# Kernel optimization log

Hardware: AMD Instinct MI355X
Metric: run time of the kernel (lower is better)

The kernel has to match this reference:

```python
import jax, jax.numpy as jnp
import numpy as np

D_MODEL = 1024
N_HEADS = 16
N_KV = 4
HD = D_MODEL // N_HEADS  # 64
N_REP = N_HEADS // N_KV
WINDOW = 128
SCALE = HD ** -0.5
B, T = 2, 2048


def _rope(x):
    # x: [B, H, T, hd]; half-split rotate_half RoPE, base 10000
    t = x.shape[2]
    hd = x.shape[-1]
    inv_freq = 1.0 / (10000.0 ** (jnp.arange(0, hd, 2, dtype=jnp.float32) / hd))
    freqs = jnp.arange(t, dtype=jnp.float32)[:, None] * inv_freq[None, :]  # [T, hd/2]
    cos = jnp.cos(freqs)[None, None]  # [1,1,T,hd/2]
    sin = jnp.sin(freqs)[None, None]
    x1, x2 = x[..., : hd // 2], x[..., hd // 2:]
    return jnp.concatenate([x1 * cos - x2 * sin, x1 * sin + x2 * cos], axis=-1)


def setup_inputs() -> dict:
    key = jax.random.key(0)
    ks = jax.random.split(key, 6)
    s = 0.02
    return {
        "query": jax.random.normal(ks[0], (B, T, D_MODEL), dtype=jnp.float32),
        "Wq": jax.random.normal(ks[1], (D_MODEL, D_MODEL), dtype=jnp.float32) * s,
        "Wk": jax.random.normal(ks[2], (N_KV * HD, D_MODEL), dtype=jnp.float32) * s,
        "Wv": jax.random.normal(ks[3], (N_KV * HD, D_MODEL), dtype=jnp.float32) * s,
        "W1": jax.random.normal(ks[4], (4 * D_MODEL, D_MODEL), dtype=jnp.float32) * s,
        "W2": jax.random.normal(ks[5], (D_MODEL, 4 * D_MODEL), dtype=jnp.float32) * s,
    }


def reference(query, Wq, Wk, Wv, W1, W2):
    b, t, _ = query.shape
    # QKV projections (nn.Linear, no bias): x @ W.T
    q = (query @ Wq.T).reshape(b, t, N_HEADS, HD).transpose(0, 2, 1, 3)  # [B,H,T,hd]
    k = (query @ Wk.T).reshape(b, t, N_KV, HD).transpose(0, 2, 1, 3)    # [B,Hkv,T,hd]
    v = (query @ Wv.T).reshape(b, t, N_KV, HD).transpose(0, 2, 1, 3)
    # Rotary embeddings on q/k (self-attention)
    q = _rope(q)
    k = _rope(k)
    # GQA: repeat kv heads (kv-head-major ordering, matches torch expand+reshape)
    k = jnp.repeat(k, N_REP, axis=1)
    v = jnp.repeat(v, N_REP, axis=1)
    # scores + causal sliding-window band mask (True = masked)
    scores = jnp.einsum("bhqd,bhkd->bhqk", q, k) * SCALE
    i = jnp.arange(t)[:, None]
    j = jnp.arange(t)[None, :]
    mask = (j > i) | (j < i - (WINDOW - 1))  # causal window of size WINDOW
    scores = jnp.where(mask[None, None], jnp.float32(-1e30), scores)
    attn = jax.nn.softmax(scores, axis=-1)
    out = jnp.einsum("bhqk,bhkd->bhqd", attn, v)
    out = out.transpose(0, 2, 1, 3).reshape(b, t, D_MODEL)
    # out_proj: Linear(d,4d) -> SiLU -> Linear(4d,d)
    h = out @ W1.T
    h = h * jax.nn.sigmoid(h)
    return h @ W2.T
```

## Files before the change

kernel.cpp:

```cpp
#include <hip/hip_runtime.h>
#include <math.h>


typedef __bf16 bf16x8 __attribute__((ext_vector_type(8)));
typedef __bf16 bf16x4 __attribute__((ext_vector_type(4)));
typedef float  f32x4  __attribute__((ext_vector_type(4)));

extern __shared__ __align__(16) char smem[];

#define GLOAD_LDS16(g, l) __builtin_amdgcn_global_load_lds(               \
    (const __attribute__((address_space(1))) void*)(g),                   \
    (__attribute__((address_space(3))) void*)(l), 16, 0, 0)

__device__ __forceinline__ unsigned pk2(float a, float b) {
    union { __bf16 h[2]; unsigned u; } t;
    t.h[0] = (__bf16)a; t.h[1] = (__bf16)b;
    return t.u;
}

__global__ __launch_bounds__(256) void MultiAttention_60722247631706_conv(
    const float* x, const float* Wq, const float* Wk, const float* Wv,
    const float* W1, const float* W2, float* out, float* ws, int phase)
{
    __bf16* xbf    = (__bf16*)(ws + 6291456);
    __bf16* wqkvbf = (__bf16*)(ws + 8388608);
    __bf16* w1bf   = (__bf16*)(ws + 10485760);
    __bf16* w2bf   = (__bf16*)(ws + 8388608);
    const int tid = threadIdx.x;

    if (phase == 5) {
        const long long total4 = 9961472 / 4;
        for (long long i4 = (long long)blockIdx.x * 256 + tid; i4 < total4;
             i4 += (long long)gridDim.x * 256) {
            const long long i = i4 * 4;
            const float* src; __bf16* dst;
            if (i < 4194304)      { src = x  + i;             dst = xbf    + i; }
            else if (i < 5242880) { src = Wq + (i - 4194304); dst = wqkvbf + (i - 4194304); }
            else if (i < 5505024) { src = Wk + (i - 5242880); dst = wqkvbf + (i - 4194304); }
            else if (i < 5767168) { src = Wv + (i - 5505024); dst = wqkvbf + (i - 4194304); }
            else                  { src = W1 + (i - 5767168); dst = w1bf   + (i - 5767168); }
            const f32x4 v = *(const f32x4*)src;
            bf16x4 o;
            o[0] = (__bf16)v[0]; o[1] = (__bf16)v[1];
            o[2] = (__bf16)v[2]; o[3] = (__bf16)v[3];
            *(bf16x4*)dst = o;
        }
    } else {
        const long long total4 = 4194304 / 4;
        for (long long i4 = (long long)blockIdx.x * 256 + tid; i4 < total4;
             i4 += (long long)gridDim.x * 256) {
            const long long i = i4 * 4;
            const f32x4 v = *(const f32x4*)(W2 + i);
            bf16x4 o;
            o[0] = (__bf16)v[0]; o[1] = (__bf16)v[1];
            o[2] = (__bf16)v[2]; o[3] = (__bf16)v[3];
            *(bf16x4*)(w2bf + i) = o;
        }
        const f32x4 z = {0.f, 0.f, 0.f, 0.f};
        for (long long i4 = (long long)blockIdx.x * 256 + tid; i4 < total4;
             i4 += (long long)gridDim.x * 256) {
            *(f32x4*)(out + i4 * 4) = z;
        }
    }
}

__global__ __launch_bounds__(256) void MultiAttention_60722247631706_attn(
    float* ws)
{
    const float* Y = ws;
    __bf16* obf = (__bf16*)(ws + 8388608);

    __bf16* Ks = (__bf16*)smem;
    __bf16* Vt = Ks + 192 * 72;

    const int qt  = blockIdx.x & 31;
    const int kvh = (blockIdx.x >> 5) & 3;
    const int b   = blockIdx.x >> 7;
    const int q0  = qt * 64;
    const int wb  = q0 - 128;

    const int tid  = threadIdx.x;
    const int w    = tid >> 6;
    const int lane = tid & 63;
    const int l16  = lane & 15;
    const int quad = lane >> 4;
    const int h    = kvh * 4 + w;

    const float* Yb = Y + (size_t)b * 2048 * 1536;

    for (int i = tid; i < 192 * 8; i += 256) {
        const int r  = i >> 3;
        const int c8 = (i & 7) * 8;
        const int j  = wb + r;
        bf16x8 kv;
        if (j >= 0) {
            const float* kp = Yb + (size_t)j * 1536 + 1024 + kvh * 64 + c8;
            const f32x4 a = *(const f32x4*)kp;
            const f32x4 c = *(const f32x4*)(kp + 4);
            kv[0] = (__bf16)a[0]; kv[1] = (__bf16)a[1];
            kv[2] = (__bf16)a[2]; kv[3] = (__bf16)a[3];
            kv[4] = (__bf16)c[0]; kv[5] = (__bf16)c[1];
            kv[6] = (__bf16)c[2]; kv[7] = (__bf16)c[3];
        } else {
            const __bf16 z = (__bf16)0.f;
            kv[0]=z; kv[1]=z; kv[2]=z; kv[3]=z; kv[4]=z; kv[5]=z; kv[6]=z; kv[7]=z;
        }
        *(bf16x8*)(Ks + r * 72 + c8) = kv;
    }
    for (int i = tid; i < 192 * 16; i += 256) {
        const int r  = i >> 4;
        const int c4 = (i & 15) * 4;
        const int j  = wb + r;
        f32x4 vv = {0.f, 0.f, 0.f, 0.f};
        if (j >= 0) vv = *(const f32x4*)(Yb + (size_t)j * 1536 + 1280 + kvh * 64 + c4);
        Vt[(c4 + 0) * 200 + r] = (__bf16)vv[0];
        Vt[(c4 + 1) * 200 + r] = (__bf16)vv[1];
        Vt[(c4 + 2) * 200 + r] = (__bf16)vv[2];
        Vt[(c4 + 3) * 200 + r] = (__bf16)vv[3];
    }

    bf16x8 qf[4][2];
#pragma unroll
    for (int qn = 0; qn < 4; ++qn)
#pragma unroll
        for (int kk = 0; kk < 2; ++kk) {
            const float* qp = Yb + (size_t)(q0 + qn * 16 + l16) * 1536
                              + h * 64 + kk * 32 + quad * 8;
            const f32x4 a = *(const f32x4*)qp;
            const f32x4 c = *(const f32x4*)(qp + 4);
            bf16x8 t;
            t[0] = (__bf16)(a[0] * 0.125f); t[1] = (__bf16)(a[1] * 0.125f);
            t[2] = (__bf16)(a[2] * 0.125f); t[3] = (__bf16)(a[3] * 0.125f);
            t[4] = (__bf16)(c[0] * 0.125f); t[5] = (__bf16)(c[1] * 0.125f);
            t[6] = (__bf16)(c[2] * 0.125f); t[7] = (__bf16)(c[3] * 0.125f);
            qf[qn][kk] = t;
        }

    __syncthreads();

    f32x4 oacc[4][4];
#pragma unroll
    for (int qm = 0; qm < 4; ++qm)
#pragma unroll
        for (int dn = 0; dn < 4; ++dn) {
            f32x4 z = {0.f, 0.f, 0.f, 0.f};
            oacc[qm][dn] = z;
        }
    float m_run[4] = {-1e30f, -1e30f, -1e30f, -1e30f};
    float l_run[4] = {0.f, 0.f, 0.f, 0.f};

    const int kclip = -wb;

    for (int kb = 0; kb < 3; ++kb) {
        f32x4 s[4][4];
#pragma unroll
        for (int km = 0; km < 4; ++km)
#pragma unroll
            for (int qn = 0; qn < 4; ++qn) {
                f32x4 z = {0.f, 0.f, 0.f, 0.f};
                s[km][qn] = z;
            }
#pragma unroll
        for (int kk = 0; kk < 2; ++kk) {
            bf16x8 kf[4];
#pragma unroll
            for (int km = 0; km < 4; ++km)
                kf[km] = *(const bf16x8*)(Ks + (kb * 64 + km * 16 + l16) * 72
                                          + kk * 32 + quad * 8);
#pragma unroll
            for (int km = 0; km < 4; ++km)
#pragma unroll
                for (int qn = 0; qn < 4; ++qn)
                    s[km][qn] = __builtin_amdgcn_mfma_f32_16x16x32_bf16(
                        kf[km], qf[qn][kk], s[km][qn], 0, 0, 0);
        }

        unsigned cu[4][4][2];
        float corr[4];
#pragma unroll
        for (int qn = 0; qn < 4; ++qn) {
            float mx = -1e30f;
#pragma unroll
            for (int km = 0; km < 4; ++km)
#pragma unroll
                for (int r = 0; r < 4; ++r) {
                    const int kl  = kb * 64 + km * 16 + quad * 4 + r;
                    const int dlt = kl - (qn * 16 + l16);
                    const bool ok = (dlt >= 1) && (dlt <= 128) && (kl >= kclip);
                    const float sv = ok ? s[km][qn][r] : -1e30f;
                    s[km][qn][r] = sv;
                    mx = fmaxf(mx, sv);
                }
            mx = fmaxf(mx, __shfl_xor(mx, 16));
            mx = fmaxf(mx, __shfl_xor(mx, 32));
            const float mnew = fmaxf(fmaxf(m_run[qn], mx), -1e20f);
            corr[qn] = expf(m_run[qn] - mnew);
            m_run[qn] = mnew;
            float rowsum = 0.f;
#pragma unroll
            for (int km = 0; km < 4; ++km) {
#pragma unroll
                for (int r = 0; r < 4; ++r) {
                    const float p = expf(s[km][qn][r] - mnew);
                    s[km][qn][r] = p;
                    rowsum += p;
                }
                cu[qn][km][0] = pk2(s[km][qn][0], s[km][qn][1]);
                cu[qn][km][1] = pk2(s[km][qn][2], s[km][qn][3]);
            }
            rowsum += __shfl_xor(rowsum, 16);
            rowsum += __shfl_xor(rowsum, 32);
            l_run[qn] = l_run[qn] * corr[qn] + rowsum;
        }

#pragma unroll
        for (int qm = 0; qm < 4; ++qm)
#pragma unroll
            for (int r = 0; r < 4; ++r) {
                const float f = __shfl(corr[qm], (lane & 48) | (quad * 4 + r));
                oacc[qm][0][r] *= f; oacc[qm][1][r] *= f;
                oacc[qm][2][r] *= f; oacc[qm][3][r] *= f;
            }

#pragma unroll
        for (int kk = 0; kk < 2; ++kk) {
            bf16x8 vf[4];
#pragma unroll
            for (int dn = 0; dn < 4; ++dn)
                vf[dn] = *(const bf16x8*)(Vt + (dn * 16 + l16) * 200
                                          + kb * 64 + kk * 32 + quad * 8);
            const int srcA = ((quad & 1) * 32) + l16;
            const int hi   = quad >> 1;
#pragma unroll
            for (int qm = 0; qm < 4; ++qm) {
                const unsigned a0 = (unsigned)__shfl((int)cu[qm][2*kk  ][0], srcA);
                const unsigned a1 = (unsigned)__shfl((int)cu[qm][2*kk  ][1], srcA);
                const unsigned b0 = (unsigned)__shfl((int)cu[qm][2*kk+1][0], srcA);
                const unsigned b1 = (unsigned)__shfl((int)cu[qm][2*kk+1][1], srcA);
                const unsigned c0 = (unsigned)__shfl((int)cu[qm][2*kk  ][0], srcA + 16);
                const unsigned c1 = (unsigned)__shfl((int)cu[qm][2*kk  ][1], srcA + 16);
                const unsigned d0 = (unsigned)__shfl((int)cu[qm][2*kk+1][0], srcA + 16);
                const unsigned d1 = (unsigned)__shfl((int)cu[qm][2*kk+1][1], srcA + 16);
                union { unsigned u[4]; bf16x8 v; } af;
                af.u[0] = hi ? b0 : a0;
                af.u[1] = hi ? b1 : a1;
                af.u[2] = hi ? d0 : c0;
                af.u[3] = hi ? d1 : c1;
#pragma unroll
                for (int dn = 0; dn < 4; ++dn)
                    oacc[qm][dn] = __builtin_amdgcn_mfma_f32_16x16x32_bf16(
                        af.v, vf[dn], oacc[qm][dn], 0, 0, 0);
            }
        }
    }

#pragma unroll
    for (int qm = 0; qm < 4; ++qm) {
        const float rl = 1.f / l_run[qm];
#pragma unroll
        for (int r = 0; r < 4; ++r) {
            const float f = __shfl(rl, (lane & 48) | (quad * 4 + r));
            const int q = q0 + qm * 16 + quad * 4 + r;
            __bf16* op = obf + ((size_t)(b * 2048 + q)) * 1024 + h * 64 + l16;
#pragma unroll
            for (int dn = 0; dn < 4; ++dn)
                op[dn * 16] = (__bf16)(oacc[qm][dn][r] * f);
        }
    }
}

__global__ __launch_bounds__(256) void MultiAttention_60722247631706_kernel(
    float* out, float* ws, int phase)
{
    float*  Y      = ws;
    __bf16* xbf    = (__bf16*)(ws + 6291456);
    __bf16* wqkvbf = (__bf16*)(ws + 8388608);
    __bf16* w1bf   = (__bf16*)(ws + 10485760);
    __bf16* obf    = (__bf16*)(ws + 8388608);
    __bf16* hbf    = (__bf16*)ws;
    __bf16* w2bf   = (__bf16*)(ws + 8388608);

    const int tid = threadIdx.x;

    __bf16* As = (__bf16*)smem;
    __bf16* Bs = As + 128 * 64;

    const __bf16* Ap; const __bf16* Bp; int lda, ldb, ntn, kbase;
    int bid = blockIdx.x;
    if (phase == 0) {
        Ap = xbf; lda = 1024; Bp = wqkvbf; ldb = 1024; ntn = 12; kbase = 0;
    } else if (phase == 3) {
        Ap = obf; lda = 1024; Bp = w1bf;   ldb = 1024; ntn = 32; kbase = 0;
    } else {
        const int ks = bid >> 8;  bid &= 255;
        Ap = hbf; lda = 4096; Bp = w2bf;   ldb = 4096; ntn = 8;
        kbase = ks * 1024;
    }
    const int K = 1024;

    const int tm   = bid / ntn;
    const int tn   = bid % ntn;
    const int w    = tid >> 6;
    const int lane = tid & 63;
    const int wr   = w >> 1;
    const int wc   = w & 1;
    const int l16  = lane & 15;
    const int quad = lane >> 4;
    const int srow = lane >> 3;
    const int sch  = ((lane & 7) ^ srow) * 8;

    const __bf16* ga0 = Ap + (size_t)(tm * 128 + w * 32 + srow) * lda + kbase + sch;
    const __bf16* gb0 = Bp + (size_t)(tn * 128 + w * 32 + srow) * ldb + kbase + sch;

    f32x4 zero = {0.f, 0.f, 0.f, 0.f};
    f32x4 acc[4][4];
#pragma unroll
    for (int mi = 0; mi < 4; ++mi)
#pragma unroll
        for (int ni = 0; ni < 4; ++ni) acc[mi][ni] = zero;

    for (int k0 = 0; k0 < K; k0 += 64) {
#pragma unroll
        for (int i = 0; i < 4; ++i) {
            GLOAD_LDS16(ga0 + (size_t)i * 8 * lda + k0, As + (w * 32 + i * 8) * 64);
            GLOAD_LDS16(gb0 + (size_t)i * 8 * ldb + k0, Bs + (w * 32 + i * 8) * 64);
        }
        __syncthreads();
#pragma unroll
        for (int kk = 0; kk < 2; ++kk) {
            const int cs = ((kk * 4 + quad) ^ (l16 & 7)) * 8;
            bf16x8 af[4], bfr[4];
#pragma unroll
            for (int mi = 0; mi < 4; ++mi)
                af[mi] = *(const bf16x8*)(As + (size_t)(wr * 64 + mi * 16 + l16) * 64 + cs);
#pragma unroll
            for (int ni = 0; ni < 4; ++ni)
                bfr[ni] = *(const bf16x8*)(Bs + (size_t)(wc * 64 + ni * 16 + l16) * 64 + cs);
#pragma unroll
            for (int mi = 0; mi < 4; ++mi)
#pragma unroll
                for (int ni = 0; ni < 4; ++ni)
                    acc[mi][ni] = __builtin_amdgcn_mfma_f32_16x16x32_bf16(
                        af[mi], bfr[ni], acc[mi][ni], 0, 0, 0);
        }
        __syncthreads();
    }

    const int mbase = tm * 128 + wr * 64;
    const int nbase = tn * 128 + wc * 64;

    if (phase == 0) {
        const bool rot = nbase < 1280;
        const float inv1 = powf(10000.f, -(float)l16 / 32.f);
        const float inv2 = powf(10000.f, -(float)(16 + l16) / 32.f);
#pragma unroll
        for (int mi = 0; mi < 4; ++mi) {
#pragma unroll
            for (int r = 0; r < 4; ++r) {
                const int m = mbase + mi * 16 + quad * 4 + r;
                const int t = m & 2047;
                float v0 = acc[mi][0][r], v1 = acc[mi][1][r];
                float v2 = acc[mi][2][r], v3 = acc[mi][3][r];
                if (rot) {
                    const float a1 = (float)t * inv1, a2 = (float)t * inv2;
                    const float c1 = cosf(a1), s1 = sinf(a1);
                    const float c2 = cosf(a2), s2 = sinf(a2);
                    const float n0 = v0 * c1 - v2 * s1;
                    const float n2 = v0 * s1 + v2 * c1;
                    const float n1 = v1 * c2 - v3 * s2;
                    const float n3 = v1 * s2 + v3 * c2;
                    v0 = n0; v1 = n1; v2 = n2; v3 = n3;
                }
                float* yp = Y + (size_t)m * 1536 + nbase + l16;
                yp[0] = v0; yp[16] = v1; yp[32] = v2; yp[48] = v3;
            }
        }
    } else if (phase == 3) {
#pragma unroll
        for (int mi = 0; mi < 4; ++mi) {
#pragma unroll
            for (int r = 0; r < 4; ++r) {
                const int m = mbase + mi * 16 + quad * 4 + r;
                __bf16* hp = hbf + (size_t)m * 4096 + nbase + l16;
#pragma unroll
                for (int ni = 0; ni < 4; ++ni) {
                    const float v = acc[mi][ni][r];
                    hp[ni * 16] = (__bf16)(v / (1.f + expf(-v)));
                }
            }
        }
    } else {
#pragma unroll
        for (int mi = 0; mi < 4; ++mi) {
#pragma unroll
            for (int r = 0; r < 4; ++r) {
                const int m = mbase + mi * 16 + quad * 4 + r;
                float* op = out + (size_t)m * 1024 + nbase + l16;
#pragma unroll
                for (int ni = 0; ni < 4; ++ni)
                    atomicAdd(op + ni * 16, acc[mi][ni][r]);
            }
        }
    }
}

extern "C" void kernel_launch(void* const* d_in, const int* in_sizes, int n_in,
                              void* d_out, int out_size, void* d_ws, size_t ws_size,
                              hipStream_t stream)
{
    const float* x  = (const float*)d_in[0];
    const float* Wq = (const float*)d_in[1];
    const float* Wk = (const float*)d_in[2];
    const float* Wv = (const float*)d_in[3];
    const float* W1 = (const float*)d_in[4];
    const float* W2 = (const float*)d_in[5];
    float* out = (float*)d_out;
    float* ws  = (float*)d_ws;

    const int GEMM_LDS = 2 * 128 * 64 * 2;
    const int ATTN_LDS = (192 * 72 + 64 * 200) * 2;

    MultiAttention_60722247631706_conv<<<2048, 256, 0, stream>>>(
        x, Wq, Wk, Wv, W1, W2, out, ws, 5);
    MultiAttention_60722247631706_kernel<<<384, 256, GEMM_LDS, stream>>>(
        out, ws, 0);
    MultiAttention_60722247631706_attn<<<256, 256, ATTN_LDS, stream>>>(ws);
    MultiAttention_60722247631706_kernel<<<1024, 256, GEMM_LDS, stream>>>(
        out, ws, 3);
    MultiAttention_60722247631706_conv<<<1024, 256, 0, stream>>>(
        x, Wq, Wk, Wv, W1, W2, out, ws, 6);
    MultiAttention_60722247631706_kernel<<<1024, 256, GEMM_LDS, stream>>>(
        out, ws, 4);
}
```

Baseline: 304.3 us.

## Split GEMM phases into dedicated FFN kernels with larger tiles and double buffering

The multi-phase GEMM kernel is split into three specialised kernels. FFN1 uses 256x256 tiles with 512 threads and double-buffered LDS staging, which raises data reuse and overlaps loads with MFMA work. FFN2 changes from a 4-way K split with 128x128 tiles to a 2-way K split with 64x128 tiles, which halves the atomicAdd traffic while keeping 1024 blocks. The cost is a 128KB LDS footprint for FFN1, which limits occupancy, plus a host-side attribute call on every launch.

After: 335.8 us. 10.3% more time.

```diff
diff --git a/kernel.cpp b/kernel.cpp
--- a/kernel.cpp
+++ b/kernel.cpp
@@ -270,36 +270,19 @@
 }
 
 __global__ __launch_bounds__(256) void MultiAttention_60722247631706_kernel(
-    float* out, float* ws, int phase)
+    float* ws)
 {
     float*  Y      = ws;
     __bf16* xbf    = (__bf16*)(ws + 6291456);
     __bf16* wqkvbf = (__bf16*)(ws + 8388608);
-    __bf16* w1bf   = (__bf16*)(ws + 10485760);
-    __bf16* obf    = (__bf16*)(ws + 8388608);
-    __bf16* hbf    = (__bf16*)ws;
-    __bf16* w2bf   = (__bf16*)(ws + 8388608);
 
     const int tid = threadIdx.x;
 
     __bf16* As = (__bf16*)smem;
     __bf16* Bs = As + 128 * 64;
 
-    const __bf16* Ap; const __bf16* Bp; int lda, ldb, ntn, kbase;
-    int bid = blockIdx.x;
-    if (phase == 0) {
-        Ap = xbf; lda = 1024; Bp = wqkvbf; ldb = 1024; ntn = 12; kbase = 0;
-    } else if (phase == 3) {
-        Ap = obf; lda = 1024; Bp = w1bf;   ldb = 1024; ntn = 32; kbase = 0;
-    } else {
-        const int ks = bid >> 8;  bid &= 255;
-        Ap = hbf; lda = 4096; Bp = w2bf;   ldb = 4096; ntn = 8;
-        kbase = ks * 1024;
-    }
-    const int K = 1024;
-
-    const int tm   = bid / ntn;
-    const int tn   = bid % ntn;
+    const int tm   = blockIdx.x / 12;
+    const int tn   = blockIdx.x % 12;
     const int w    = tid >> 6;
     const int lane = tid & 63;
     const int wr   = w >> 1;
@@ -309,8 +292,8 @@
     const int srow = lane >> 3;
     const int sch  = ((lane & 7) ^ srow) * 8;
 
-    const __bf16* ga0 = Ap + (size_t)(tm * 128 + w * 32 + srow) * lda + kbase + sch;
-    const __bf16* gb0 = Bp + (size_t)(tn * 128 + w * 32 + srow) * ldb + kbase + sch;
+    const __bf16* ga0 = xbf    + (size_t)(tm * 128 + w * 32 + srow) * 1024 + sch;
+    const __bf16* gb0 = wqkvbf + (size_t)(tn * 128 + w * 32 + srow) * 1024 + sch;
 
     f32x4 zero = {0.f, 0.f, 0.f, 0.f};
     f32x4 acc[4][4];
@@ -319,11 +302,11 @@
 #pragma unroll
         for (int ni = 0; ni < 4; ++ni) acc[mi][ni] = zero;
 
-    for (int k0 = 0; k0 < K; k0 += 64) {
+    for (int k0 = 0; k0 < 1024; k0 += 64) {
 #pragma unroll
         for (int i = 0; i < 4; ++i) {
-            GLOAD_LDS16(ga0 + (size_t)i * 8 * lda + k0, As + (w * 32 + i * 8) * 64);
-            GLOAD_LDS16(gb0 + (size_t)i * 8 * ldb + k0, Bs + (w * 32 + i * 8) * 64);
+            GLOAD_LDS16(ga0 + (size_t)i * 8 * 1024 + k0, As + (w * 32 + i * 8) * 64);
+            GLOAD_LDS16(gb0 + (size_t)i * 8 * 1024 + k0, Bs + (w * 32 + i * 8) * 64);
         }
         __syncthreads();
 #pragma unroll
@@ -349,57 +332,205 @@
     const int mbase = tm * 128 + wr * 64;
     const int nbase = tn * 128 + wc * 64;
 
-    if (phase == 0) {
-        const bool rot = nbase < 1280;
-        const float inv1 = powf(10000.f, -(float)l16 / 32.f);
-        const float inv2 = powf(10000.f, -(float)(16 + l16) / 32.f);
-#pragma unroll
-        for (int mi = 0; mi < 4; ++mi) {
-#pragma unroll
-            for (int r = 0; r < 4; ++r) {
-                const int m = mbase + mi * 16 + quad * 4 + r;
-                const int t = m & 2047;
-                float v0 = acc[mi][0][r], v1 = acc[mi][1][r];
-                float v2 = acc[mi][2][r], v3 = acc[mi][3][r];
-                if (rot) {
-                    const float a1 = (float)t * inv1, a2 = (float)t * inv2;
-                    const float c1 = cosf(a1), s1 = sinf(a1);
-                    const float c2 = cosf(a2), s2 = sinf(a2);
-                    const float n0 = v0 * c1 - v2 * s1;
-                    const float n2 = v0 * s1 + v2 * c1;
-                    const float n1 = v1 * c2 - v3 * s2;
-                    const float n3 = v1 * s2 + v3 * c2;
-                    v0 = n0; v1 = n1; v2 = n2; v3 = n3;
-                }
-                float* yp = Y + (size_t)m * 1536 + nbase + l16;
-                yp[0] = v0; yp[16] = v1; yp[32] = v2; yp[48] = v3;
+    const bool rot = nbase < 1280;
+    const float inv1 = powf(10000.f, -(float)l16 / 32.f);
+    const float inv2 = powf(10000.f, -(float)(16 + l16) / 32.f);
+#pragma unroll
+    for (int mi = 0; mi < 4; ++mi) {
+#pragma unroll
+        for (int r = 0; r < 4; ++r) {
+            const int m = mbase + mi * 16 + quad * 4 + r;
+            const int t = m & 2047;
+            float v0 = acc[mi][0][r], v1 = acc[mi][1][r];
+            float v2 = acc[mi][2][r], v3 = acc[mi][3][r];
+            if (rot) {
+                const float a1 = (float)t * inv1, a2 = (float)t * inv2;
+                const float c1 = cosf(a1), s1 = sinf(a1);
+                const float c2 = cosf(a2), s2 = sinf(a2);
+                const float n0 = v0 * c1 - v2 * s1;
+                const float n2 = v0 * s1 + v2 * c1;
+                const float n1 = v1 * c2 - v3 * s2;
+                const float n3 = v1 * s2 + v3 * c2;
+                v0 = n0; v1 = n1; v2 = n2; v3 = n3;
             }
-        }
-    } else if (phase == 3) {
-#pragma unroll
-        for (int mi = 0; mi < 4; ++mi) {
-#pragma unroll
-            for (int r = 0; r < 4; ++r) {
-                const int m = mbase + mi * 16 + quad * 4 + r;
-                __bf16* hp = hbf + (size_t)m * 4096 + nbase + l16;
-#pragma unroll
-                for (int ni = 0; ni < 4; ++ni) {
-                    const float v = acc[mi][ni][r];
-                    hp[ni * 16] = (__bf16)(v / (1.f + expf(-v)));
-                }
+            float* yp = Y + (size_t)m * 1536 + nbase + l16;
+            yp[0] = v0; yp[16] = v1; yp[32] = v2; yp[48] = v3;
+        }
+    }
+}
+
+template <bool DBUF>
+__global__ __launch_bounds__(512, 2) void MultiAttention_60722247631706_ffn1(
+    float* ws)
+{
+    __bf16* obf  = (__bf16*)(ws + 8388608);
+    __bf16* w1bf = (__bf16*)(ws + 10485760);
+    __bf16* hbf  = (__bf16*)ws;
+
+    const int tid  = threadIdx.x;
+    const int w    = tid >> 6;
+    const int lane = tid & 63;
+    const int wr   = w >> 2;
+    const int wc   = w & 3;
+    const int l16  = lane & 15;
+    const int quad = lane >> 4;
+    const int srow = lane >> 3;
+    const int sch  = ((lane & 7) ^ srow) * 8;
+
+    const int tm = blockIdx.x >> 4;
+    const int tn = blockIdx.x & 15;
+
+    __bf16* S = (__bf16*)smem;
+
+    const __bf16* ga0 = obf  + (size_t)(tm * 256 + w * 32 + srow) * 1024 + sch;
+    const __bf16* gb0 = w1bf + (size_t)(tn * 256 + w * 32 + srow) * 1024 + sch;
+
+    f32x4 acc[8][4];
+#pragma unroll
+    for (int mi = 0; mi < 8; ++mi)
+#pragma unroll
+        for (int ni = 0; ni < 4; ++ni) {
+            f32x4 z = {0.f, 0.f, 0.f, 0.f};
+            acc[mi][ni] = z;
+        }
+
+    auto stage = [&](int p, int k0) {
+        __bf16* As = S + p * 32768;
+        __bf16* Bs = As + 16384;
+#pragma unroll
+        for (int i = 0; i < 4; ++i) {
+            GLOAD_LDS16(ga0 + (size_t)i * 8 * 1024 + k0, As + (w * 32 + i * 8) * 64);
+            GLOAD_LDS16(gb0 + (size_t)i * 8 * 1024 + k0, Bs + (w * 32 + i * 8) * 64);
+        }
+    };
+    auto compute = [&](int p) {
+        const __bf16* As = S + p * 32768;
+        const __bf16* Bs = As + 16384;
+#pragma unroll
+        for (int kk = 0; kk < 2; ++kk) {
+            const int cs = ((kk * 4 + quad) ^ (l16 & 7)) * 8;
+            bf16x8 af[8], bfr[4];
+#pragma unroll
+            for (int mi = 0; mi < 8; ++mi)
+                af[mi] = *(const bf16x8*)(As + (size_t)(wr * 128 + mi * 16 + l16) * 64 + cs);
+#pragma unroll
+            for (int ni = 0; ni < 4; ++ni)
+                bfr[ni] = *(const bf16x8*)(Bs + (size_t)(wc * 64 + ni * 16 + l16) * 64 + cs);
+#pragma unroll
+            for (int mi = 0; mi < 8; ++mi)
+#pragma unroll
+                for (int ni = 0; ni < 4; ++ni)
+                    acc[mi][ni] = __builtin_amdgcn_mfma_f32_16x16x32_bf16(
+                        af[mi], bfr[ni], acc[mi][ni], 0, 0, 0);
+        }
+    };
+
+    if constexpr (DBUF) {
+        stage(0, 0);
+        __syncthreads();
+        int cur = 0;
+        for (int t = 0; t < 16; ++t) {
+            if (t < 15) stage(cur ^ 1, (t + 1) * 64);
+            compute(cur);
+            __syncthreads();
+            cur ^= 1;
+        }
+    } else {
+        for (int t = 0; t < 16; ++t) {
+            stage(0, t * 64);
+            __syncthreads();
+            compute(0);
+            __syncthreads();
+        }
+    }
+
+#pragma unroll
+    for (int mi = 0; mi < 8; ++mi) {
+#pragma unroll
+        for (int r = 0; r < 4; ++r) {
+            const int m = tm * 256 + wr * 128 + mi * 16 + quad * 4 + r;
+            __bf16* hp = hbf + (size_t)m * 4096 + tn * 256 + wc * 64 + l16;
+#pragma unroll
+            for (int ni = 0; ni < 4; ++ni) {
+                const float v = acc[mi][ni][r];
+                hp[ni * 16] = (__bf16)(v / (1.f + expf(-v)));
             }
         }
-    } else {
-#pragma unroll
-        for (int mi = 0; mi < 4; ++mi) {
-#pragma unroll
-            for (int r = 0; r < 4; ++r) {
-                const int m = mbase + mi * 16 + quad * 4 + r;
-                float* op = out + (size_t)m * 1024 + nbase + l16;
+    }
+}
+
+__global__ __launch_bounds__(256) void MultiAttention_60722247631706_ffn2(
+    float* out, float* ws)
+{
+    __bf16* hbf  = (__bf16*)ws;
+    __bf16* w2bf = (__bf16*)(ws + 8388608);
+
+    int bid = blockIdx.x;
+    const int ks = bid >> 9;  bid &= 511;
+    const int tm = bid >> 3;
+    const int tn = bid & 7;
+    const int kbase = ks * 2048;
+
+    const int tid  = threadIdx.x;
+    const int w    = tid >> 6;
+    const int lane = tid & 63;
+    const int wr   = w >> 1;
+    const int wc   = w & 1;
+    const int l16  = lane & 15;
+    const int quad = lane >> 4;
+    const int srow = lane >> 3;
+    const int sch  = ((lane & 7) ^ srow) * 8;
+
+    __bf16* As = (__bf16*)smem;
+    __bf16* Bs = As + 64 * 64;
+
+    const __bf16* ga0 = hbf  + (size_t)(tm * 64  + w * 16 + srow) * 4096 + kbase + sch;
+    const __bf16* gb0 = w2bf + (size_t)(tn * 128 + w * 32 + srow) * 4096 + kbase + sch;
+
+    f32x4 zero = {0.f, 0.f, 0.f, 0.f};
+    f32x4 acc[2][4];
+#pragma unroll
+    for (int mi = 0; mi < 2; ++mi)
+#pragma unroll
+        for (int ni = 0; ni < 4; ++ni) acc[mi][ni] = zero;
+
+    for (int k0 = 0; k0 < 2048; k0 += 64) {
+#pragma unroll
+        for (int i = 0; i < 2; ++i)
+            GLOAD_LDS16(ga0 + (size_t)i * 8 * 4096 + k0, As + (w * 16 + i * 8) * 64);
+#pragma unroll
+        for (int i = 0; i < 4; ++i)
+            GLOAD_LDS16(gb0 + (size_t)i * 8 * 4096 + k0, Bs + (w * 32 + i * 8) * 64);
+        __syncthreads();
+#pragma unroll
+        for (int kk = 0; kk < 2; ++kk) {
+            const int cs = ((kk * 4 + quad) ^ (l16 & 7)) * 8;
+            bf16x8 af[2], bfr[4];
+#pragma unroll
+            for (int mi = 0; mi < 2; ++mi)
+                af[mi] = *(const bf16x8*)(As + (size_t)(wr * 32 + mi * 16 + l16) * 64 + cs);
+#pragma unroll
+            for (int ni = 0; ni < 4; ++ni)
+                bfr[ni] = *(const bf16x8*)(Bs + (size_t)(wc * 64 + ni * 16 + l16) * 64 + cs);
+#pragma unroll
+            for (int mi = 0; mi < 2; ++mi)
 #pragma unroll
                 for (int ni = 0; ni < 4; ++ni)
-                    atomicAdd(op + ni * 16, acc[mi][ni][r]);
-            }
+                    acc[mi][ni] = __builtin_amdgcn_mfma_f32_16x16x32_bf16(
+                        af[mi], bfr[ni], acc[mi][ni], 0, 0, 0);
+        }
+        __syncthreads();
+    }
+
+#pragma unroll
+    for (int mi = 0; mi < 2; ++mi) {
+#pragma unroll
+        for (int r = 0; r < 4; ++r) {
+            const int m = tm * 64 + wr * 32 + mi * 16 + quad * 4 + r;
+            float* op = out + (size_t)m * 1024 + tn * 128 + wc * 64 + l16;
+#pragma unroll
+            for (int ni = 0; ni < 4; ++ni)
+                atomicAdd(op + ni * 16, acc[mi][ni][r]);
         }
     }
 }
@@ -419,16 +550,23 @@
 
     const int GEMM_LDS = 2 * 128 * 64 * 2;
     const int ATTN_LDS = (192 * 72 + 64 * 200) * 2;
+    const int FFN1_LDS = 2 * 2 * 256 * 64 * 2;
+    const int FFN2_LDS = (64 + 128) * 64 * 2;
 
     MultiAttention_60722247631706_conv<<<2048, 256, 0, stream>>>(
         x, Wq, Wk, Wv, W1, W2, out, ws, 5);
-    MultiAttention_60722247631706_kernel<<<384, 256, GEMM_LDS, stream>>>(
-        out, ws, 0);
+    MultiAttention_60722247631706_kernel<<<384, 256, GEMM_LDS, stream>>>(ws);
     MultiAttention_60722247631706_attn<<<256, 256, ATTN_LDS, stream>>>(ws);
-    MultiAttention_60722247631706_kernel<<<1024, 256, GEMM_LDS, stream>>>(
-        out, ws, 3);
+    hipError_t e = hipFuncSetAttribute(
+        reinterpret_cast<const void*>(MultiAttention_60722247631706_ffn1<true>),
+        hipFuncAttributeMaxDynamicSharedMemorySize, FFN1_LDS);
+    if (e == hipSuccess) {
+        MultiAttention_60722247631706_ffn1<true><<<256, 512, FFN1_LDS, stream>>>(ws);
+    } else {
+        (void)hipGetLastError();
+        MultiAttention_60722247631706_ffn1<false><<<256, 512, FFN1_LDS / 2, stream>>>(ws);
+    }
     MultiAttention_60722247631706_conv<<<1024, 256, 0, stream>>>(
         x, Wq, Wk, Wv, W1, W2, out, ws, 6);
-    MultiAttention_60722247631706_kernel<<<1024, 256, GEMM_LDS, stream>>>(
-        out, ws, 4);
-}
+    MultiAttention_60722247631706_ffn2<<<1024, 256, FFN2_LDS, stream>>>(out, ws);
+}
```
